# Kernel optimization log

Measured on AMD Instinct MI355X. Metric: run time of the kernel, lower is better.

Reference implementation:

```python
import jax, jax.numpy as jnp
import numpy as np

B, C, N = 4, 128, 8192
CQK = C // 4  # query/key projection dim = out_channels // 4


def setup_inputs() -> dict:
    key = jax.random.key(0)
    ks = jax.random.split(key, 9)
    s_in = 1.0 / np.sqrt(C)
    return {
        "x": jax.random.normal(ks[0], (B, C, N), dtype=jnp.float32),
        "xyz": jax.random.normal(ks[1], (B, N, 3), dtype=jnp.float32),
        "Wq": jax.random.normal(ks[2], (CQK, C), dtype=jnp.float32) * s_in,
        "bq": jax.random.normal(ks[3], (CQK,), dtype=jnp.float32) * 0.01,
        "Wk": jax.random.normal(ks[4], (CQK, C), dtype=jnp.float32) * s_in,
        "bk": jax.random.normal(ks[5], (CQK,), dtype=jnp.float32) * 0.01,
        "Wv": jax.random.normal(ks[6], (C, C), dtype=jnp.float32) * s_in,
        "bv": jax.random.normal(ks[7], (C,), dtype=jnp.float32) * 0.01,
        "gamma": jax.random.normal(ks[8], (1,), dtype=jnp.float32) * 0.1,
    }


def reference(x, xyz, Wq, bq, Wk, bk, Wv, bv, gamma):
    # 1x1 Conv1d == per-point linear projection over channels
    q = jnp.einsum('oc,bcn->bon', Wq, x) + bq[None, :, None]   # (B, CQK, N)
    k = jnp.einsum('oc,bcn->bon', Wk, x) + bk[None, :, None]   # (B, CQK, N)
    v = jnp.einsum('oc,bcn->bon', Wv, x) + bv[None, :, None]   # (B, C, N)

    # energy[b, n, m] = <q[:, n], k[:, m]>
    energy = jnp.einsum('bcn,bcm->bnm', q, k)                  # (B, N, N)

    # positional correlation bias: normalize coords per point, cosine-sim matrix
    xyz_bcn = jnp.swapaxes(xyz, 1, 2)                          # (B, 3, N)
    xyz_norm = xyz_bcn / (jnp.linalg.norm(xyz_bcn, axis=1, keepdims=True) + 1e-8)
    pos_corr = jnp.einsum('bcn,bcm->bnm', xyz_norm, xyz_norm)  # (B, N, N)
    energy = energy + 0.1 * pos_corr

    attention = jax.nn.softmax(energy, axis=-1)                # rowwise over m

    # out[b, c, n] = sum_m v[b, c, m] * attention[b, n, m]
    out = jnp.einsum('bcm,bnm->bcn', v, attention)             # (B, C, N)
    return gamma * out + x
```

## Files before the change

### kernel.cpp

```cpp
#include <hip/hip_runtime.h>

#define NPTS 8192
#define NB 4
#define NCH 128
#define DQK 48
#define TK 64
#define SPLIT 4
#define KEYS_PER (NPTS / SPLIT)
#define ROUNDS (KEYS_PER / TK)
#define SH2 28.853901f
#define LOG2E 1.4426950408889634f

typedef unsigned short ushort_t;
typedef unsigned int uint_t;
typedef __attribute__((ext_vector_type(8))) short bf16x8;
typedef __attribute__((ext_vector_type(4))) float f32x4;
typedef __attribute__((ext_vector_type(16))) float f32x16;

static __device__ __forceinline__ ushort_t f2bf(float x) {
  union { float f; uint_t u; } v; v.f = x;
  uint_t r = v.u + 0x7fffu + ((v.u >> 16) & 1u);
  return (ushort_t)(r >> 16);
}
static __device__ __forceinline__ float bf2f(ushort_t u) {
  union { uint_t i; float f; } v; v.i = ((uint_t)u) << 16; return v.f;
}
static __device__ __forceinline__ int sig16(int n) {
  int g2 = (n >> 2) & 3;
  return (g2 == 1 || g2 == 2) ? (n ^ 0xC) : n;
}

typedef __attribute__((address_space(1))) void void_g;
typedef __attribute__((address_space(3))) void void_l;
static __device__ __forceinline__ void gload_lds16(const ushort_t* g, ushort_t* l) {
  __builtin_amdgcn_global_load_lds((void_g*)(ushort_t*)g, (void_l*)l, 16, 0, 0);
}

__global__ __launch_bounds__(256, 2)
void projm_kernel(const float* __restrict__ x, const float* __restrict__ xyz,
                  const float* __restrict__ Wq, const float* __restrict__ bq,
                  const float* __restrict__ Wk, const float* __restrict__ bk,
                  const float* __restrict__ Wv, const float* __restrict__ bv,
                  ushort_t* __restrict__ Qb, ushort_t* __restrict__ Kb,
                  ushort_t* __restrict__ Vt) {
  const int tid = threadIdx.x;
  const int lane = tid & 63, wv = tid >> 6;
  const int l31 = lane & 31, h = lane >> 5;
  const int b = blockIdx.y, z = blockIdx.z;
  const int n = blockIdx.x * 128 + wv * 32 + l31;

  const float* W; const float* bias; float sc;
  if (z == 0)      { W = Wq; bias = bq; sc = LOG2E; }
  else if (z == 1) { W = Wk; bias = bk; sc = 1.f; }
  else { W = Wv + (size_t)(z - 2) * 32 * 128; bias = bv + (z - 2) * 32; sc = 1.f; }

  bf16x8 af[8];
#pragma unroll
  for (int ks = 0; ks < 8; ++ks) {
    const float* wr = W + l31 * 128 + ks * 16 + h * 8;
    float4 w0 = *(const float4*)wr;
    float4 w1 = *(const float4*)(wr + 4);
    union { ushort_t u[8]; bf16x8 v; } p;
    p.u[0] = f2bf(w0.x * sc); p.u[1] = f2bf(w0.y * sc);
    p.u[2] = f2bf(w0.z * sc); p.u[3] = f2bf(w0.w * sc);
    p.u[4] = f2bf(w1.x * sc); p.u[5] = f2bf(w1.y * sc);
    p.u[6] = f2bf(w1.z * sc); p.u[7] = f2bf(w1.w * sc);
    af[ks] = p.v;
  }

  f32x16 S;
#pragma unroll
  for (int r = 0; r < 16; ++r)
    S[r] = bias[(r & 3) + 8 * (r >> 2) + 4 * h] * sc;

  const float* xb = x + (size_t)b * NCH * NPTS + n;
#pragma unroll
  for (int ks = 0; ks < 8; ++ks) {
    const float* xc = xb + (size_t)(ks * 16 + h * 8) * NPTS;
    union { ushort_t u[8]; bf16x8 v; } p;
#pragma unroll
    for (int j = 0; j < 8; ++j) p.u[j] = f2bf(xc[(size_t)j * NPTS]);
    S = __builtin_amdgcn_mfma_f32_32x32x16_bf16(af[ks], p.v, S, 0, 0, 0);
  }

  if (z <= 1) {
    ushort_t* dst = (z == 0 ? Qb : Kb) + ((size_t)b * NPTS + n) * DQK;
#pragma unroll
    for (int r = 0; r < 16; ++r)
      dst[(r & 3) + 8 * (r >> 2) + 4 * h] = f2bf(S[r]);
    float xa = xyz[((size_t)b * NPTS + n) * 3 + 0];
    float xc = xyz[((size_t)b * NPTS + n) * 3 + 1];
    float xd = xyz[((size_t)b * NPTS + n) * 3 + 2];
    float rn = 0.31622776601683794f * sc /
               (sqrtf(xa * xa + xc * xc + xd * xd) + 1e-8f);
    union { ushort_t u[16]; bf16x8 v[2]; } t;
#pragma unroll
    for (int j = 0; j < 16; ++j) t.u[j] = 0;
    t.u[0] = f2bf(xa * rn); t.u[1] = f2bf(xc * rn); t.u[2] = f2bf(xd * rn);
    *(bf16x8*)(dst + 32) = t.v[0];
    *(bf16x8*)(dst + 40) = t.v[1];
  } else {
    const int np = (n & ~15) | sig16(n & 15);
    const int c0 = (z - 2) * 32;
#pragma unroll
    for (int r = 0; r < 16; ++r)
      Vt[((size_t)b * NCH + c0 + (r & 3) + 8 * (r >> 2) + 4 * h) * NPTS + np] =
          f2bf(S[r]);
  }
}

__global__ __launch_bounds__(512, 2)
void attn32_kernel(const ushort_t* __restrict__ Qb, const ushort_t* __restrict__ Kb,
                   const ushort_t* __restrict__ Vt,
                   ushort_t* __restrict__ PACC, float* __restrict__ PL) {
  __shared__ __align__(16) ushort_t L[2][22][512];
  const int tid = threadIdx.x;
  const int lane = tid & 63, w = tid >> 6;
  const int l31 = lane & 31, h = lane >> 5;

  const int lin = blockIdx.x;
  const int bs = lin & 15;
  const int b = bs & 3, sseg = bs >> 2;
  const int qblk = lin >> 4;
  const int q0w = qblk * 512 + w * 64;
  const int m00 = sseg * KEYS_PER;

  bf16x8 qf[2][3];
#pragma unroll
  for (int g = 0; g < 2; ++g)
#pragma unroll
    for (int c = 0; c < 3; ++c)
      qf[g][c] = *(const bf16x8*)(Qb + ((size_t)b * NPTS + q0w + g * 32 + l31) * DQK +
                                  c * 16 + h * 8);

  const ushort_t* gp[3];
  int fid[3], adv[3];
  const int nf = (w < 6) ? 3 : 2;
  for (int i = 0; i < nf; ++i) {
    int fi = w + 8 * i;
    fid[i] = fi;
    if (fi < 6) {
      int kb = fi / 3, c = fi - kb * 3;
      gp[i] = Kb + ((size_t)b * NPTS + m00 + kb * 32 + l31) * DQK + c * 16 + h * 8;
      adv[i] = TK * DQK;
    } else {
      int vi = fi - 6, fch = vi >> 2, kk = vi & 3;
      gp[i] = Vt + ((size_t)b * NCH + fch * 32 + l31) * NPTS + m00 + kk * 16 + h * 8;
      adv[i] = TK;
    }
  }

  f32x16 O[2][4];
#pragma unroll
  for (int g = 0; g < 2; ++g)
#pragma unroll
    for (int f = 0; f < 4; ++f) O[g][f] = (f32x16)(0.f);
  float lsum0 = 0.f, lsum1 = 0.f;

  for (int i = 0; i < nf; ++i) gload_lds16(gp[i], &L[0][fid[i]][0]);

#pragma unroll 1
  for (int t = 0; t < ROUNDS; ++t) {
    __syncthreads();
    const int cur = t & 1;
    if (t + 1 < ROUNDS) {
      for (int i = 0; i < nf; ++i) {
        gp[i] += adv[i];
        gload_lds16(gp[i], &L[cur ^ 1][fid[i]][0]);
      }
    }

#pragma unroll
    for (int kb = 0; kb < 2; ++kb) {
      bf16x8 kf0 = *(const bf16x8*)(&L[cur][kb * 3 + 0][0] + lane * 8);
      bf16x8 kf1 = *(const bf16x8*)(&L[cur][kb * 3 + 1][0] + lane * 8);
      bf16x8 kf2 = *(const bf16x8*)(&L[cur][kb * 3 + 2][0] + lane * 8);

      uint_t pk[2][8];
#pragma unroll
      for (int g = 0; g < 2; ++g) {
        f32x16 S = __builtin_amdgcn_mfma_f32_32x32x16_bf16(kf0, qf[g][0], (f32x16)(0.f), 0, 0, 0);
        S = __builtin_amdgcn_mfma_f32_32x32x16_bf16(kf1, qf[g][1], S, 0, 0, 0);
        S = __builtin_amdgcn_mfma_f32_32x32x16_bf16(kf2, qf[g][2], S, 0, 0, 0);
        float p[16];
        float ts = 0.f;
#pragma unroll
        for (int r = 0; r < 16; ++r) {
          p[r] = __builtin_amdgcn_exp2f(S[r] - SH2);
          ts += p[r];
        }
        if (g == 0) lsum0 += ts; else lsum1 += ts;
#pragma unroll
        for (int i = 0; i < 8; ++i)
          pk[g][i] = __builtin_amdgcn_perm(__float_as_uint(p[2 * i + 1]),
                                           __float_as_uint(p[2 * i]), 0x07060302u);
      }

#pragma unroll
      for (int kkl = 0; kkl < 2; ++kkl) {
        bf16x8 A[2];
#pragma unroll
        for (int g = 0; g < 2; ++g) {
          union { uint_t u[4]; bf16x8 v; } au;
          au.u[0] = pk[g][4 * kkl + 0];
          au.u[1] = pk[g][4 * kkl + 1];
          au.u[2] = pk[g][4 * kkl + 2];
          au.u[3] = pk[g][4 * kkl + 3];
          A[g] = au.v;
        }
#pragma unroll
        for (int f = 0; f < 4; ++f) {
          bf16x8 vf = *(const bf16x8*)(&L[cur][6 + f * 4 + kb * 2 + kkl][0] + lane * 8);
          O[0][f] = __builtin_amdgcn_mfma_f32_32x32x16_bf16(A[0], vf, O[0][f], 0, 0, 0);
          O[1][f] = __builtin_amdgcn_mfma_f32_32x32x16_bf16(A[1], vf, O[1][f], 0, 0, 0);
        }
      }
    }
  }

  lsum0 += __shfl_xor(lsum0, 32);
  lsum1 += __shfl_xor(lsum1, 32);
  const size_t pbase = (((size_t)bs * 16 + qblk) * 8 + w) * 2;
#pragma unroll
  for (int g = 0; g < 2; ++g) {
#pragma unroll
    for (int f = 0; f < 4; ++f) {
      union { ushort_t u[16]; bf16x8 v[2]; } pu;
#pragma unroll
      for (int r = 0; r < 16; ++r) pu.u[r] = f2bf(O[g][f][r]);
      size_t idx = ((pbase + g) * 4 + f) * 1024 + (size_t)lane * 16;
      *(bf16x8*)(PACC + idx) = pu.v[0];
      *(bf16x8*)(PACC + idx + 8) = pu.v[1];
    }
    if (lane < 32)
      PL[(size_t)bs * NPTS + q0w + g * 32 + lane] = (g == 0) ? lsum0 : lsum1;
  }
}

__global__ __launch_bounds__(256, 4)
void merge4_kernel(const ushort_t* __restrict__ PACC, const float* __restrict__ PL,
                   const float* __restrict__ x, const float* __restrict__ gamma,
                   float* __restrict__ out) {
  __shared__ float Linv[256];
  const int tid = threadIdx.x;
  const int qblk2 = blockIdx.x, b = blockIdx.y, f = blockIdx.z;
  const int q0 = qblk2 * 256;

  float Ls = 0.f;
#pragma unroll
  for (int s = 0; s < 4; ++s)
    Ls += PL[(size_t)(s * 4 + b) * NPTS + q0 + tid];
  Linv[tid] = gamma[0] / Ls;
  __syncthreads();

  const int ww = tid >> 6, lane = tid & 63, l31 = lane & 31, h = lane >> 5;
  const int ch = f * 32 + l31;
  const float* xrow = x + ((size_t)b * NCH + ch) * NPTS + q0;
  float* orow = out + ((size_t)b * NCH + ch) * NPTS + q0;

#pragma unroll
  for (int g = 0; g < 2; ++g) {
    float acc[16];
#pragma unroll
    for (int r = 0; r < 16; ++r) acc[r] = 0.f;
#pragma unroll
    for (int s = 0; s < 4; ++s) {
      size_t idx = (((((size_t)(s * 4 + b) * 16 + (qblk2 >> 1)) * 8 +
                      (qblk2 & 1) * 4 + ww) * 2 + g) * 4 + f) * 1024 +
                   (size_t)lane * 16;
      bf16x8 a0 = *(const bf16x8*)(PACC + idx);
      bf16x8 a1 = *(const bf16x8*)(PACC + idx + 8);
#pragma unroll
      for (int r = 0; r < 8; ++r) {
        acc[r] += bf2f((ushort_t)a0[r]);
        acc[8 + r] += bf2f((ushort_t)a1[r]);
      }
    }
    const int qb = ww * 64 + g * 32;
#pragma unroll
    for (int rr = 0; rr < 4; ++rr) {
      int q = qb + 8 * rr + 4 * h;
      f32x4 xv = *(const f32x4*)(xrow + q);
      f32x4 o;
#pragma unroll
      for (int i = 0; i < 4; ++i) o[i] = acc[rr * 4 + i] * Linv[q + i] + xv[i];
      *(f32x4*)(orow + q) = o;
    }
  }
}

extern "C" void kernel_launch(void* const* d_in, const int* in_sizes, int n_in,
                              void* d_out, int out_size, void* d_ws,
                              size_t ws_size, hipStream_t stream) {
  const float* x     = (const float*)d_in[0];
  const float* xyz   = (const float*)d_in[1];
  const float* Wq    = (const float*)d_in[2];
  const float* bq    = (const float*)d_in[3];
  const float* Wk    = (const float*)d_in[4];
  const float* bk    = (const float*)d_in[5];
  const float* Wv    = (const float*)d_in[6];
  const float* bv    = (const float*)d_in[7];
  const float* gamma = (const float*)d_in[8];
  float* out = (float*)d_out;

  const size_t BN = (size_t)NB * NPTS;
  ushort_t* Qb = (ushort_t*)d_ws;
  ushort_t* Kb = Qb + BN * DQK;
  ushort_t* Vt = Kb + BN * DQK;
  ushort_t* PACC = Vt + BN * NCH;
  float* PL = (float*)(PACC + (size_t)16 * 16 * 8 * 2 * 4 * 1024);

  projm_kernel<<<dim3(NPTS / 128, NB, 6), 256, 0, stream>>>(
      x, xyz, Wq, bq, Wk, bk, Wv, bv, Qb, Kb, Vt);
  attn32_kernel<<<256, 512, 0, stream>>>(Qb, Kb, Vt, PACC, PL);
  merge4_kernel<<<dim3(32, NB, 4), 256, 0, stream>>>(PACC, PL, x, gamma, out);
  (void)in_sizes; (void)n_in; (void)out_size; (void)ws_size;
}
```

Baseline: 204.3 us.

## Precompute bf16 weight fragments and load x once for all six projections

Adds a tiny kernel that converts the Q/K/V weights to bf16 MFMA fragment layout, along with pre-scaled biases. The projection kernel then loads and converts each x tile once and loops over all six output groups, instead of launching six z-slices that each re-read x. This cuts redundant global reads of x and repeated weight conversion. In exchange it adds an extra kernel launch and leaves fewer, serialized blocks in the projection stage.

```diff
diff --git a/kernel.cpp b/kernel.cpp
--- a/kernel.cpp
+++ b/kernel.cpp
@@ -36,43 +36,41 @@
   __builtin_amdgcn_global_load_lds((void_g*)(ushort_t*)g, (void_l*)l, 16, 0, 0);
 }
 
-__global__ __launch_bounds__(256, 2)
-void projm_kernel(const float* __restrict__ x, const float* __restrict__ xyz,
-                  const float* __restrict__ Wq, const float* __restrict__ bq,
+__global__ __launch_bounds__(512, 1)
+void wprep_kernel(const float* __restrict__ Wq, const float* __restrict__ bq,
                   const float* __restrict__ Wk, const float* __restrict__ bk,
                   const float* __restrict__ Wv, const float* __restrict__ bv,
-                  ushort_t* __restrict__ Qb, ushort_t* __restrict__ Kb,
-                  ushort_t* __restrict__ Vt) {
+                  ushort_t* __restrict__ Wb, float* __restrict__ bias_pre) {
+  const int z = blockIdx.x;
+  const int ks = threadIdx.x >> 6;
+  const int lane = threadIdx.x & 63;
+  const int l31 = lane & 31, h = lane >> 5;
+  const float* W = (z == 0) ? Wq : (z == 1) ? Wk : (Wv + (size_t)(z - 2) * 32 * 128);
+  const float sc = (z == 0) ? LOG2E : 1.0f;
+  const float* wr = W + l31 * 128 + ks * 16 + h * 8;
+  union { ushort_t u[8]; bf16x8 v; } p;
+#pragma unroll
+  for (int j = 0; j < 8; ++j) p.u[j] = f2bf(wr[j] * sc);
+  *(bf16x8*)(Wb + ((size_t)(z * 8 + ks) * 64 + lane) * 8) = p.v;
+  if (z == 0 && threadIdx.x < 192) {
+    int i = threadIdx.x;
+    bias_pre[i] = (i < 32) ? bq[i] * LOG2E : (i < 64) ? bk[i - 32] : bv[i - 64];
+  }
+}
+
+__global__ __launch_bounds__(256, 4)
+void projm2_kernel(const float* __restrict__ x, const float* __restrict__ xyz,
+                   const ushort_t* __restrict__ Wb,
+                   const float* __restrict__ bias_pre,
+                   ushort_t* __restrict__ Qb, ushort_t* __restrict__ Kb,
+                   ushort_t* __restrict__ Vt) {
   const int tid = threadIdx.x;
   const int lane = tid & 63, wv = tid >> 6;
   const int l31 = lane & 31, h = lane >> 5;
-  const int b = blockIdx.y, z = blockIdx.z;
+  const int b = blockIdx.y;
   const int n = blockIdx.x * 128 + wv * 32 + l31;
 
-  const float* W; const float* bias; float sc;
-  if (z == 0)      { W = Wq; bias = bq; sc = LOG2E; }
-  else if (z == 1) { W = Wk; bias = bk; sc = 1.f; }
-  else { W = Wv + (size_t)(z - 2) * 32 * 128; bias = bv + (z - 2) * 32; sc = 1.f; }
-
-  bf16x8 af[8];
-#pragma unroll
-  for (int ks = 0; ks < 8; ++ks) {
-    const float* wr = W + l31 * 128 + ks * 16 + h * 8;
-    float4 w0 = *(const float4*)wr;
-    float4 w1 = *(const float4*)(wr + 4);
-    union { ushort_t u[8]; bf16x8 v; } p;
-    p.u[0] = f2bf(w0.x * sc); p.u[1] = f2bf(w0.y * sc);
-    p.u[2] = f2bf(w0.z * sc); p.u[3] = f2bf(w0.w * sc);
-    p.u[4] = f2bf(w1.x * sc); p.u[5] = f2bf(w1.y * sc);
-    p.u[6] = f2bf(w1.z * sc); p.u[7] = f2bf(w1.w * sc);
-    af[ks] = p.v;
-  }
-
-  f32x16 S;
-#pragma unroll
-  for (int r = 0; r < 16; ++r)
-    S[r] = bias[(r & 3) + 8 * (r >> 2) + 4 * h] * sc;
-
+  bf16x8 bfr[8];
   const float* xb = x + (size_t)b * NCH * NPTS + n;
 #pragma unroll
   for (int ks = 0; ks < 8; ++ks) {
@@ -80,32 +78,46 @@
     union { ushort_t u[8]; bf16x8 v; } p;
 #pragma unroll
     for (int j = 0; j < 8; ++j) p.u[j] = f2bf(xc[(size_t)j * NPTS]);
-    S = __builtin_amdgcn_mfma_f32_32x32x16_bf16(af[ks], p.v, S, 0, 0, 0);
-  }
-
-  if (z <= 1) {
-    ushort_t* dst = (z == 0 ? Qb : Kb) + ((size_t)b * NPTS + n) * DQK;
+    bfr[ks] = p.v;
+  }
+
+  float xa = xyz[((size_t)b * NPTS + n) * 3 + 0];
+  float xc2 = xyz[((size_t)b * NPTS + n) * 3 + 1];
+  float xd = xyz[((size_t)b * NPTS + n) * 3 + 2];
+  float rinv = 1.0f / (sqrtf(xa * xa + xc2 * xc2 + xd * xd) + 1e-8f);
+
+#pragma unroll 1
+  for (int z = 0; z < 6; ++z) {
+    f32x16 S;
 #pragma unroll
     for (int r = 0; r < 16; ++r)
-      dst[(r & 3) + 8 * (r >> 2) + 4 * h] = f2bf(S[r]);
-    float xa = xyz[((size_t)b * NPTS + n) * 3 + 0];
-    float xc = xyz[((size_t)b * NPTS + n) * 3 + 1];
-    float xd = xyz[((size_t)b * NPTS + n) * 3 + 2];
-    float rn = 0.31622776601683794f * sc /
-               (sqrtf(xa * xa + xc * xc + xd * xd) + 1e-8f);
-    union { ushort_t u[16]; bf16x8 v[2]; } t;
-#pragma unroll
-    for (int j = 0; j < 16; ++j) t.u[j] = 0;
-    t.u[0] = f2bf(xa * rn); t.u[1] = f2bf(xc * rn); t.u[2] = f2bf(xd * rn);
-    *(bf16x8*)(dst + 32) = t.v[0];
-    *(bf16x8*)(dst + 40) = t.v[1];
-  } else {
-    const int np = (n & ~15) | sig16(n & 15);
-    const int c0 = (z - 2) * 32;
-#pragma unroll
-    for (int r = 0; r < 16; ++r)
-      Vt[((size_t)b * NCH + c0 + (r & 3) + 8 * (r >> 2) + 4 * h) * NPTS + np] =
-          f2bf(S[r]);
+      S[r] = bias_pre[z * 32 + (r & 3) + 8 * (r >> 2) + 4 * h];
+#pragma unroll
+    for (int ks = 0; ks < 8; ++ks) {
+      bf16x8 af = *(const bf16x8*)(Wb + ((size_t)(z * 8 + ks) * 64 + lane) * 8);
+      S = __builtin_amdgcn_mfma_f32_32x32x16_bf16(af, bfr[ks], S, 0, 0, 0);
+    }
+    if (z <= 1) {
+      float sc = (z == 0) ? LOG2E : 1.0f;
+      ushort_t* dst = (z == 0 ? Qb : Kb) + ((size_t)b * NPTS + n) * DQK;
+#pragma unroll
+      for (int r = 0; r < 16; ++r)
+        dst[(r & 3) + 8 * (r >> 2) + 4 * h] = f2bf(S[r]);
+      float rn = 0.31622776601683794f * sc * rinv;
+      union { ushort_t u[16]; bf16x8 v[2]; } t;
+#pragma unroll
+      for (int j = 0; j < 16; ++j) t.u[j] = 0;
+      t.u[0] = f2bf(xa * rn); t.u[1] = f2bf(xc2 * rn); t.u[2] = f2bf(xd * rn);
+      *(bf16x8*)(dst + 32) = t.v[0];
+      *(bf16x8*)(dst + 40) = t.v[1];
+    } else {
+      const int np = (n & ~15) | sig16(n & 15);
+      const int c0 = (z - 2) * 32;
+#pragma unroll
+      for (int r = 0; r < 16; ++r)
+        Vt[((size_t)b * NCH + c0 + (r & 3) + 8 * (r >> 2) + 4 * h) * NPTS + np] =
+            f2bf(S[r]);
+    }
   }
 }
 
@@ -309,9 +321,12 @@
   ushort_t* Vt = Kb + BN * DQK;
   ushort_t* PACC = Vt + BN * NCH;
   float* PL = (float*)(PACC + (size_t)16 * 16 * 8 * 2 * 4 * 1024);
-
-  projm_kernel<<<dim3(NPTS / 128, NB, 6), 256, 0, stream>>>(
-      x, xyz, Wq, bq, Wk, bk, Wv, bv, Qb, Kb, Vt);
+  ushort_t* Wb = (ushort_t*)(PL + 16 * BN / 2);
+  float* bias_pre = (float*)(Wb + 6 * 8 * 64 * 8);
+
+  wprep_kernel<<<6, 512, 0, stream>>>(Wq, bq, Wk, bk, Wv, bv, Wb, bias_pre);
+  projm2_kernel<<<dim3(NPTS / 128, NB), 256, 0, stream>>>(
+      x, xyz, Wb, bias_pre, Qb, Kb, Vt);
   attn32_kernel<<<256, 512, 0, stream>>>(Qb, Kb, Vt, PACC, PL);
   merge4_kernel<<<dim3(32, NB, 4), 256, 0, stream>>>(PACC, PL, x, gamma, out);
   (void)in_sizes; (void)n_in; (void)out_size; (void)ws_size;
```

Result: no change. 201.3 us (-1.5%).
